# Kernel tuning notes

Measured on AMD Instinct MI355X. Metric: run time of the kernel, lower is better.

Reference implementation:

```python
import jax, jax.numpy as jnp
import numpy as np

M, A, E, H = 2048, 64, 128, 256
NUM_BOND_TYPES, NUM_ATOM_TYPES = 4, 118

def setup_inputs() -> dict:
    key = jax.random.key(0)
    ks = jax.random.split(key, 12)
    s = 0.02
    return {
        'node_rep': jax.random.normal(ks[0], (M, A, H), jnp.float32),
        'edge_index': jax.random.randint(ks[1], (M, 2, E), 0, A, jnp.int32),
        'bond_type_target': jax.random.randint(ks[2], (M, E), 0, NUM_BOND_TYPES, jnp.int32),
        'atom_type_target': jax.random.randint(ks[3], (M, A), 0, NUM_ATOM_TYPES, jnp.int32),
        'Wp1': jax.random.normal(ks[4], (H, H), jnp.float32) * s, 'bp1': jnp.zeros((H,), jnp.float32),
        'Wp2': jax.random.normal(ks[5], (H, H), jnp.float32) * s, 'bp2': jnp.zeros((H,), jnp.float32),
        'Wb1': jax.random.normal(ks[6], (2 * H, H), jnp.float32) * s, 'bb1': jnp.zeros((H,), jnp.float32),
        'Wb2': jax.random.normal(ks[7], (H, NUM_BOND_TYPES), jnp.float32) * s, 'bb2': jnp.zeros((NUM_BOND_TYPES,), jnp.float32),
        'Wa1': jax.random.normal(ks[8], (H, H), jnp.float32) * s, 'ba1': jnp.zeros((H,), jnp.float32),
        'Wa2': jax.random.normal(ks[9], (H, NUM_ATOM_TYPES), jnp.float32) * s, 'ba2': jnp.zeros((NUM_ATOM_TYPES,), jnp.float32),
    }

def _mlp(x, W1, b1, W2, b2):
    return jnp.maximum(x @ W1 + b1, 0.0) @ W2 + b2

def reference(node_rep, edge_index, bond_type_target, atom_type_target,
              Wp1, bp1, Wp2, bp2, Wb1, bb1, Wb2, bb2, Wa1, ba1, Wa2, ba2):
    # bond_if_proj: per-atom 2-layer MLP (dropout=0 -> identity)  [M,A,H]
    proj = _mlp(node_rep, Wp1, bp1, Wp2, bp2)
    # gather bond endpoint reps: index_select over atoms per molecule  [M,E,H]
    start = jnp.take_along_axis(proj, edge_index[:, 0, :, None], axis=1)
    end = jnp.take_along_axis(proj, edge_index[:, 1, :, None], axis=1)
    bt_in = jnp.concatenate([start, end], axis=-1)            # [M,E,2H]
    bt_logits = _mlp(bt_in, Wb1, bb1, Wb2, bb2)               # [M,E,4]
    bt_logp = jax.nn.log_softmax(bt_logits, axis=-1)
    # per-molecule mean CE averaged over molecules == global mean (equal sizes)
    bond_type_loss = -jnp.mean(jnp.take_along_axis(bt_logp, bond_type_target[..., None], axis=-1))
    bond_type_acc = jnp.mean((jnp.argmax(bt_logits, axis=-1) == bond_type_target).astype(jnp.float32))
    # atom type classifier on raw node reps  [M,A,118]
    at_logits = _mlp(node_rep, Wa1, ba1, Wa2, ba2)
    at_logp = jax.nn.log_softmax(at_logits, axis=-1)
    atom_type_loss = -jnp.mean(jnp.take_along_axis(at_logp, atom_type_target[..., None], axis=-1))
    atom_type_acc = jnp.mean((jnp.argmax(at_logits, axis=-1) == atom_type_target).astype(jnp.float32))
    loss = 0.5 * bond_type_loss + 0.5 * atom_type_loss
    return loss, bond_type_acc, atom_type_acc
```

## Files before the change

### kernel.cpp

```cpp
#include <hip/hip_runtime.h>
#include <hip/hip_bf16.h>

typedef __bf16 bf16x8 __attribute__((ext_vector_type(8)));
typedef float f32x16 __attribute__((ext_vector_type(16)));

__device__ inline unsigned short f2bf(float f) {
  __hip_bfloat16 h = __float2bfloat16(f);
  return *reinterpret_cast<unsigned short*>(&h);
}
__device__ inline unsigned pack2bf(float a, float b) {
  return (unsigned)f2bf(a) | ((unsigned)f2bf(b) << 16);
}
__device__ inline uint2 pack4bf(float a, float b, float c, float d) {
  uint2 r; r.x = pack2bf(a, b); r.y = pack2bf(c, d); return r;
}
__device__ inline bf16x8 as_bf16x8(uint4 v) { return __builtin_bit_cast(bf16x8, v); }
__device__ inline float bitf(unsigned u) { return __builtin_bit_cast(float, u); }
__device__ inline f32x16 mfma16(bf16x8 a, bf16x8 b, f32x16 c) {
  return __builtin_amdgcn_mfma_f32_32x32x16_bf16(a, b, c, 0, 0, 0);
}

#define BADDR(XB, R, KK)                                                       \
  ((XB) + (((((R) * 32 + l31) << 9) + ((KK) << 5) + (h << 4)) ^ swz))

#define GEMM22(XB, WPTR, CW_)                                                  \
  {                                                                            \
    const unsigned char* wb_ = (const unsigned char*)(WPTR) +                  \
                               (((CW_) + l31) << 5) + (h << 4);                \
    acc00 = zero; acc01 = zero; acc10 = zero; acc11 = zero;                    \
    bf16x8 pB0 = *(const bf16x8*)BADDR(XB, 0, 0);                              \
    bf16x8 pB1 = *(const bf16x8*)BADDR(XB, 1, 0);                              \
    uint4 pA0 = *(const uint4*)(wb_ + 0);                                      \
    uint4 pA1 = *(const uint4*)(wb_ + 1024);                                   \
    _Pragma("clang loop unroll(disable)")                                      \
    for (int kk = 0; kk < 16; kk += 2) {                                       \
      bf16x8 qB0 = *(const bf16x8*)BADDR(XB, 0, kk + 1);                       \
      bf16x8 qB1 = *(const bf16x8*)BADDR(XB, 1, kk + 1);                       \
      uint4 qA0 = *(const uint4*)(wb_ + ((kk + 1) << 13));                     \
      uint4 qA1 = *(const uint4*)(wb_ + ((kk + 1) << 13) + 1024);              \
      acc00 = mfma16(as_bf16x8(pA0), pB0, acc00);                              \
      acc10 = mfma16(as_bf16x8(pA1), pB0, acc10);                              \
      acc01 = mfma16(as_bf16x8(pA0), pB1, acc01);                              \
      acc11 = mfma16(as_bf16x8(pA1), pB1, acc11);                              \
      if (kk + 2 < 16) {                                                       \
        pB0 = *(const bf16x8*)BADDR(XB, 0, kk + 2);                            \
        pB1 = *(const bf16x8*)BADDR(XB, 1, kk + 2);                            \
        pA0 = *(const uint4*)(wb_ + ((kk + 2) << 13));                         \
        pA1 = *(const uint4*)(wb_ + ((kk + 2) << 13) + 1024);                  \
      }                                                                        \
      acc00 = mfma16(as_bf16x8(qA0), qB0, acc00);                              \
      acc10 = mfma16(as_bf16x8(qA1), qB0, acc10);                              \
      acc01 = mfma16(as_bf16x8(qA0), qB1, acc01);                              \
      acc11 = mfma16(as_bf16x8(qA1), qB1, acc11);                              \
    }                                                                          \
  }

#define WB22(DB, ACC, R, C, CW_, BIASPTR)                                      \
  _Pragma("unroll")                                                            \
  for (int g = 0; g < 4; ++g) {                                                \
    int xr_ = (R) * 32 + l31;                                                  \
    int col = (CW_) + (C) * 32 + g * 8 + h * 4;                                \
    float4 bb = *(const float4*)((BIASPTR) + col);                             \
    float v0 = fmaxf(ACC[4 * g + 0] + bb.x, 0.f);                              \
    float v1 = fmaxf(ACC[4 * g + 1] + bb.y, 0.f);                              \
    float v2 = fmaxf(ACC[4 * g + 2] + bb.z, 0.f);                              \
    float v3 = fmaxf(ACC[4 * g + 3] + bb.w, 0.f);                              \
    int off = ((xr_ << 9) + (col << 1)) ^ ((xr_ & 7) << 4);                    \
    *(uint2*)((DB) + off) = pack4bf(v0, v1, v2, v3);                           \
  }

#define WB22R(DB, ACC, R, C, CW_)                                              \
  _Pragma("unroll")                                                            \
  for (int g = 0; g < 4; ++g) {                                                \
    int xr_ = (R) * 32 + l31;                                                  \
    int col = (CW_) + (C) * 32 + g * 8 + h * 4;                                \
    int off = ((xr_ << 9) + (col << 1)) ^ ((xr_ & 7) << 4);                    \
    *(uint2*)((DB) + off) = pack4bf(ACC[4 * g + 0], ACC[4 * g + 1],            \
                                    ACC[4 * g + 2], ACC[4 * g + 3]);           \
  }

#define STAGE_X(DST, SRC)                                                      \
  _Pragma("unroll")                                                            \
  for (int it = 0; it < 8; ++it) {                                             \
    int lb = (it * 256 + tid) * 16;                                            \
    int d_ = lb ^ (((lb >> 9) & 7) << 4);                                      \
    const float4* s4 = (const float4*)((SRC) + (lb >> 1));                     \
    float4 f0 = s4[0], f1 = s4[1];                                             \
    uint4 v_ = { pack2bf(f0.x, f0.y), pack2bf(f0.z, f0.w),                     \
                 pack2bf(f1.x, f1.y), pack2bf(f1.z, f1.w) };                   \
    *(uint4*)((DST) + d_) = v_;                                                \
  }

__global__ __launch_bounds__(256) void k_pack(
    const float* __restrict__ wp1, const float* __restrict__ wa1,
    const float* __restrict__ wa2,
    unsigned short* __restrict__ dp1, unsigned short* __restrict__ da1,
    unsigned short* __restrict__ da2, float* __restrict__ accum)
{
  int b = blockIdx.x, tid = threadIdx.x;
  if (b == 0 && tid < 8) accum[tid] = 0.f;
  const float* src; unsigned short* dst; int e, logN, Nreal;
  if (b < 256)       { src = wp1; dst = dp1; e = b * 256 + tid;          logN = 8; Nreal = 256; }
  else if (b < 512)  { src = wa1; dst = da1; e = (b - 256) * 256 + tid;  logN = 8; Nreal = 256; }
  else               { src = wa2; dst = da2; e = (b - 512) * 256 + tid;  logN = 7; Nreal = 118; }
  int dk = e & 15;
  int rest = e >> 4;
  int n = rest & ((1 << logN) - 1);
  int kk = rest >> logN;
  int k = kk * 16 + dk;
  float v = (n < Nreal) ? src[k * Nreal + n] : 0.f;
  dst[e] = f2bf(v);
}

__global__ __launch_bounds__(256) void k_fold(
    const float* __restrict__ wp2, const float* __restrict__ wb1,
    const float* __restrict__ bp2, const float* __restrict__ bb1,
    unsigned short* __restrict__ dct, unsigned short* __restrict__ dcb,
    float* __restrict__ bias_e)
{
  int b = blockIdx.x, n = threadIdx.x;
  if (b < 512) {
    int k = b & 255;
    int off = (b < 256) ? 0 : 256;
    float s = 0.f;
    for (int t = 0; t < 256; ++t)
      s += wp2[k * 256 + t] * wb1[(t + off) * 256 + n];
    unsigned short* dst = (b < 256) ? dct : dcb;
    dst[((k >> 4) * 256 + n) * 16 + (k & 15)] = f2bf(s);
  } else {
    float s = bb1[n];
    for (int t = 0; t < 256; ++t)
      s += bp2[t] * (wb1[t * 256 + n] + wb1[(256 + t) * 256 + n]);
    bias_e[n] = s;
  }
}

__global__ __launch_bounds__(256, 2) void k_mol(
    const float* __restrict__ node, const int* __restrict__ eidx,
    const int* __restrict__ btt, const int* __restrict__ att,
    const unsigned short* __restrict__ wp1p, const float* __restrict__ bp1,
    const unsigned short* __restrict__ wctp, const unsigned short* __restrict__ wcbp,
    const float* __restrict__ bias_e, const float* __restrict__ wb2,
    const float* __restrict__ bb2,
    const unsigned short* __restrict__ wa1p, const float* __restrict__ ba1,
    const unsigned short* __restrict__ wa2p, const float* __restrict__ ba2,
    float* __restrict__ accum)
{
  __shared__ __align__(16) unsigned char bufA[32768];
  __shared__ __align__(16) unsigned char bufB[32768];
  __shared__ float s_bias[256];
  __shared__ float4 s_wb2[256];
  __shared__ float s_b2a[128];
  __shared__ float s_red[8];
  const int tid = threadIdx.x;
  const int lane = tid & 63;
  const int w = tid >> 6;
  const int l31 = lane & 31;
  const int h = lane >> 5;
  const int swz = (l31 & 7) << 4;
  const int CW = w * 64;
  const int m = blockIdx.x;

  STAGE_X(bufA, node + (long)m * 16384);
  s_bias[tid] = bias_e[tid];
  s_wb2[tid] = ((const float4*)wb2)[tid];
  if (tid < 128) s_b2a[tid] = (tid < 118) ? ba2[tid] : 0.f;
  __syncthreads();

  f32x16 zero = {};
  f32x16 acc00, acc01, acc10, acc11;

  GEMM22(bufA, wa1p, CW);
  WB22(bufB, acc00, 0, 0, CW, ba1);
  WB22(bufB, acc10, 0, 1, CW, ba1);
  WB22(bufB, acc01, 1, 0, CW, ba1);
  WB22(bufB, acc11, 1, 1, CW, ba1);
  __syncthreads();

  f32x16 accL0 = zero, accL1 = zero;
  {
    const int cw2 = w * 32;
    const unsigned char* wb_ = (const unsigned char*)wa2p +
                               ((cw2 + l31) << 5) + (h << 4);
    bf16x8 pB0 = *(const bf16x8*)BADDR(bufB, 0, 0);
    bf16x8 pB1 = *(const bf16x8*)BADDR(bufB, 1, 0);
    uint4 pA = *(const uint4*)(wb_);
    _Pragma("clang loop unroll(disable)")
    for (int kk = 0; kk < 16; kk += 2) {
      bf16x8 qB0 = *(const bf16x8*)BADDR(bufB, 0, kk + 1);
      bf16x8 qB1 = *(const bf16x8*)BADDR(bufB, 1, kk + 1);
      uint4 qA = *(const uint4*)(wb_ + ((kk + 1) << 12));
      accL0 = mfma16(as_bf16x8(pA), pB0, accL0);
      accL1 = mfma16(as_bf16x8(pA), pB1, accL1);
      if (kk + 2 < 16) {
        pB0 = *(const bf16x8*)BADDR(bufB, 0, kk + 2);
        pB1 = *(const bf16x8*)BADDR(bufB, 1, kk + 2);
        pA = *(const uint4*)(wb_ + ((kk + 2) << 12));
      }
      accL0 = mfma16(as_bf16x8(qA), qB0, accL0);
      accL1 = mfma16(as_bf16x8(qA), qB1, accL1);
    }
  }
  __syncthreads();

  {
    const int cw2 = w * 32;
    #pragma unroll
    for (int q = 0; q < 16; ++q) {
      int col = cw2 + (q & 3) + 8 * (q >> 2) + 4 * h;
      if (col < 118) {
        float bv = s_b2a[col];
        int r0 = l31, r1 = 32 + l31;
        *(float*)(bufB + ((r0 << 9) + (((col << 2)) ^ ((r0 & 7) << 4)))) = accL0[q] + bv;
        *(float*)(bufB + ((r1 << 9) + (((col << 2)) ^ ((r1 & 7) << 4)))) = accL1[q] + bv;
      }
    }
  }
  __syncthreads();

  {
    const int row = tid >> 2, g4 = tid & 3;
    const int t = att[m * 64 + row];
    const unsigned char* lr = bufB + (row << 9);
    const int rswz = (row & 7) << 4;
    const int c0 = g4 * 30;
    const int cend = (g4 == 3) ? 118 : c0 + 30;
    float mx = -3.0e38f; int am = 127;
    for (int c = c0; c < cend; ++c) {
      float v = *(const float*)(lr + (((c << 2)) ^ rswz));
      if (v > mx) { mx = v; am = c; }
    }
    float mo = __shfl_xor(mx, 1); int amo = __shfl_xor(am, 1);
    if (mo > mx || (mo == mx && amo < am)) { mx = mo; am = amo; }
    mo = __shfl_xor(mx, 2); amo = __shfl_xor(am, 2);
    if (mo > mx || (mo == mx && amo < am)) { mx = mo; am = amo; }
    float s = 0.f, vt = 0.f;
    for (int c = c0; c < cend; ++c) {
      float v = *(const float*)(lr + (((c << 2)) ^ rswz));
      s += __expf(v - mx);
      if (c == t) vt = v;
    }
    s += __shfl_xor(s, 1); s += __shfl_xor(s, 2);
    vt += __shfl_xor(vt, 1); vt += __shfl_xor(vt, 2);
    float ce = 0.f, cc = 0.f;
    if (g4 == 0) { ce = __logf(s) + mx - vt; cc = (am == t) ? 1.f : 0.f; }
    #pragma unroll
    for (int d = 1; d < 64; d <<= 1) { ce += __shfl_xor(ce, d); cc += __shfl_xor(cc, d); }
    if (lane == 0) { s_red[w * 2] = ce; s_red[w * 2 + 1] = cc; }
  }
  __syncthreads();
  if (tid == 0) {
    atomicAdd(accum + 2, s_red[0] + s_red[2] + s_red[4] + s_red[6]);
    atomicAdd(accum + 3, s_red[1] + s_red[3] + s_red[5] + s_red[7]);
  }

  GEMM22(bufA, wp1p, CW);
  WB22(bufB, acc00, 0, 0, CW, bp1);
  WB22(bufB, acc10, 0, 1, CW, bp1);
  WB22(bufB, acc01, 1, 0, CW, bp1);
  WB22(bufB, acc11, 1, 1, CW, bp1);
  __syncthreads();

  GEMM22(bufB, wctp, CW);
  WB22R(bufA, acc00, 0, 0, CW);
  WB22R(bufA, acc10, 0, 1, CW);
  WB22R(bufA, acc01, 1, 0, CW);
  WB22R(bufA, acc11, 1, 1, CW);
  GEMM22(bufB, wcbp, CW);
  const int es = eidx[m * 256 + (tid >> 1)];
  const int ed = eidx[m * 256 + 128 + (tid >> 1)];
  const int etg = btt[m * 128 + (tid >> 1)];
  const float b20 = bb2[0], b21 = bb2[1], b22 = bb2[2], b23 = bb2[3];
  __syncthreads();
  WB22R(bufB, acc00, 0, 0, CW);
  WB22R(bufB, acc10, 0, 1, CW);
  WB22R(bufB, acc01, 1, 0, CW);
  WB22R(bufB, acc11, 1, 1, CW);
  __syncthreads();

  {
    const int hf = tid & 1;
    float lg0 = 0.f, lg1 = 0.f, lg2 = 0.f, lg3 = 0.f;
    #pragma unroll
    for (int j = 0; j < 16; ++j) {
      int c0 = hf * 128 + j * 8;
      int offS = ((es << 9) + (c0 << 1)) ^ ((es & 7) << 4);
      int offD = ((ed << 9) + (c0 << 1)) ^ ((ed & 7) << 4);
      uint4 us = *(const uint4*)(bufA + offS);
      uint4 ud = *(const uint4*)(bufB + offD);
      const unsigned* pu = (const unsigned*)&us;
      const unsigned* pv = (const unsigned*)&ud;
      #pragma unroll
      for (int q = 0; q < 4; ++q) {
        unsigned ua = pu[q], ub = pv[q];
        int c = c0 + 2 * q;
        float hlo = bitf(ua << 16) + bitf(ub << 16) + s_bias[c];
        float hhi = bitf(ua & 0xffff0000u) + bitf(ub & 0xffff0000u) + s_bias[c + 1];
        hlo = fmaxf(hlo, 0.f); hhi = fmaxf(hhi, 0.f);
        float4 w0 = s_wb2[c], w1 = s_wb2[c + 1];
        lg0 = fmaf(hlo, w0.x, fmaf(hhi, w1.x, lg0));
        lg1 = fmaf(hlo, w0.y, fmaf(hhi, w1.y, lg1));
        lg2 = fmaf(hlo, w0.z, fmaf(hhi, w1.z, lg2));
        lg3 = fmaf(hlo, w0.w, fmaf(hhi, w1.w, lg3));
      }
    }
    lg0 += __shfl_xor(lg0, 1); lg1 += __shfl_xor(lg1, 1);
    lg2 += __shfl_xor(lg2, 1); lg3 += __shfl_xor(lg3, 1);
    float ce = 0.f, cc = 0.f;
    if (hf == 0) {
      float l0 = lg0 + b20, l1 = lg1 + b21, l2 = lg2 + b22, l3 = lg3 + b23;
      int t = etg;
      int am = 0; float mx = l0;
      if (l1 > mx) { mx = l1; am = 1; }
      if (l2 > mx) { mx = l2; am = 2; }
      if (l3 > mx) { mx = l3; am = 3; }
      float s = __expf(l0 - mx) + __expf(l1 - mx) + __expf(l2 - mx) + __expf(l3 - mx);
      float lt = (t == 0) ? l0 : (t == 1) ? l1 : (t == 2) ? l2 : l3;
      ce = __logf(s) + mx - lt;
      cc = (am == t) ? 1.f : 0.f;
    }
    #pragma unroll
    for (int d = 1; d < 64; d <<= 1) { ce += __shfl_xor(ce, d); cc += __shfl_xor(cc, d); }
    if (lane == 0) { s_red[w * 2] = ce; s_red[w * 2 + 1] = cc; }
    __syncthreads();
    if (tid == 0) {
      atomicAdd(accum + 0, s_red[0] + s_red[2] + s_red[4] + s_red[6]);
      atomicAdd(accum + 1, s_red[1] + s_red[3] + s_red[5] + s_red[7]);
    }
  }
}

__global__ __launch_bounds__(64) void k_final(const float* __restrict__ accum,
                                              float* __restrict__ out)
{
  if (threadIdx.x == 0) {
    float bce = accum[0] / 262144.f;
    float bcc = accum[1] / 262144.f;
    float ace = accum[2] / 131072.f;
    float acc_ = accum[3] / 131072.f;
    out[0] = 0.5f * bce + 0.5f * ace;
    out[1] = bcc;
    out[2] = acc_;
  }
}

extern "C" void kernel_launch(void* const* d_in, const int* in_sizes, int n_in,
                              void* d_out, int out_size, void* d_ws, size_t ws_size,
                              hipStream_t stream)
{
  const float* node = (const float*)d_in[0];
  const int* eidx   = (const int*)d_in[1];
  const int* btt    = (const int*)d_in[2];
  const int* att    = (const int*)d_in[3];
  const float* Wp1 = (const float*)d_in[4];
  const float* bp1 = (const float*)d_in[5];
  const float* Wp2 = (const float*)d_in[6];
  const float* bp2 = (const float*)d_in[7];
  const float* Wb1 = (const float*)d_in[8];
  const float* bb1 = (const float*)d_in[9];
  const float* Wb2 = (const float*)d_in[10];
  const float* bb2 = (const float*)d_in[11];
  const float* Wa1 = (const float*)d_in[12];
  const float* ba1 = (const float*)d_in[13];
  const float* Wa2 = (const float*)d_in[14];
  const float* ba2 = (const float*)d_in[15];

  char* ws = (char*)d_ws;
  float* accum = (float*)ws;
  unsigned short* dp1 = (unsigned short*)(ws + 256);
  unsigned short* da1 = (unsigned short*)(ws + 131328);
  unsigned short* da2 = (unsigned short*)(ws + 262400);
  unsigned short* dct = (unsigned short*)(ws + 327936);
  unsigned short* dcb = (unsigned short*)(ws + 459008);
  float* bias_e       = (float*)(ws + 590080);

  k_pack<<<640, 256, 0, stream>>>(Wp1, Wa1, Wa2, dp1, da1, da2, accum);
  k_fold<<<513, 256, 0, stream>>>(Wp2, Wb1, bp2, bb1, dct, dcb, bias_e);
  k_mol<<<2048, 256, 0, stream>>>(node, eidx, btt, att, dp1, bp1, dct, dcb,
                                  bias_e, Wb2, bb2, da1, ba1, da2, ba2, accum);
  k_final<<<1, 64, 0, stream>>>(accum, (float*)d_out);
}
```

Measured before the change: 195.4 us.

## Fuse paired GEMMs sharing the same LDS input into dual-weight MFMA loops

Merges the atom-head first layer with the projection first layer, and the two bond-endpoint projections, into one loop each. Each loop reads the shared LDS activation tile once and applies two weight matrices, so activation reads and loop overhead are halved and more independent MFMAs are in flight. The raw node tile in bufA is overwritten early by the projection output, which removes one GEMM phase and one barrier from the schedule. The cost is twice as many live accumulator registers (eight 16-float accumulators), which may reduce occupancy or cause spills.

```diff
diff --git a/kernel.cpp b/kernel.cpp
--- a/kernel.cpp
+++ b/kernel.cpp
@@ -23,35 +23,52 @@
 #define BADDR(XB, R, KK)                                                       \
   ((XB) + (((((R) * 32 + l31) << 9) + ((KK) << 5) + (h << 4)) ^ swz))
 
-#define GEMM22(XB, WPTR, CW_)                                                  \
+#define GEMMM(XB, W1PTR, W2PTR, CW_)                                           \
   {                                                                            \
-    const unsigned char* wb_ = (const unsigned char*)(WPTR) +                  \
+    const unsigned char* w1_ = (const unsigned char*)(W1PTR) +                 \
                                (((CW_) + l31) << 5) + (h << 4);                \
-    acc00 = zero; acc01 = zero; acc10 = zero; acc11 = zero;                    \
+    const unsigned char* w2_ = (const unsigned char*)(W2PTR) +                 \
+                               (((CW_) + l31) << 5) + (h << 4);                \
+    u00 = zero; u01 = zero; u10 = zero; u11 = zero;                            \
+    v00 = zero; v01 = zero; v10 = zero; v11 = zero;                            \
     bf16x8 pB0 = *(const bf16x8*)BADDR(XB, 0, 0);                              \
     bf16x8 pB1 = *(const bf16x8*)BADDR(XB, 1, 0);                              \
-    uint4 pA0 = *(const uint4*)(wb_ + 0);                                      \
-    uint4 pA1 = *(const uint4*)(wb_ + 1024);                                   \
+    uint4 pA0 = *(const uint4*)(w1_ + 0);                                      \
+    uint4 pA1 = *(const uint4*)(w1_ + 1024);                                   \
+    uint4 pC0 = *(const uint4*)(w2_ + 0);                                      \
+    uint4 pC1 = *(const uint4*)(w2_ + 1024);                                   \
     _Pragma("clang loop unroll(disable)")                                      \
     for (int kk = 0; kk < 16; kk += 2) {                                       \
       bf16x8 qB0 = *(const bf16x8*)BADDR(XB, 0, kk + 1);                       \
       bf16x8 qB1 = *(const bf16x8*)BADDR(XB, 1, kk + 1);                       \
-      uint4 qA0 = *(const uint4*)(wb_ + ((kk + 1) << 13));                     \
-      uint4 qA1 = *(const uint4*)(wb_ + ((kk + 1) << 13) + 1024);              \
-      acc00 = mfma16(as_bf16x8(pA0), pB0, acc00);                              \
-      acc10 = mfma16(as_bf16x8(pA1), pB0, acc10);                              \
-      acc01 = mfma16(as_bf16x8(pA0), pB1, acc01);                              \
-      acc11 = mfma16(as_bf16x8(pA1), pB1, acc11);                              \
+      uint4 qA0 = *(const uint4*)(w1_ + ((kk + 1) << 13));                     \
+      uint4 qA1 = *(const uint4*)(w1_ + ((kk + 1) << 13) + 1024);              \
+      uint4 qC0 = *(const uint4*)(w2_ + ((kk + 1) << 13));                     \
+      uint4 qC1 = *(const uint4*)(w2_ + ((kk + 1) << 13) + 1024);              \
+      u00 = mfma16(as_bf16x8(pA0), pB0, u00);                                  \
+      u10 = mfma16(as_bf16x8(pA1), pB0, u10);                                  \
+      u01 = mfma16(as_bf16x8(pA0), pB1, u01);                                  \
+      u11 = mfma16(as_bf16x8(pA1), pB1, u11);                                  \
+      v00 = mfma16(as_bf16x8(pC0), pB0, v00);                                  \
+      v10 = mfma16(as_bf16x8(pC1), pB0, v10);                                  \
+      v01 = mfma16(as_bf16x8(pC0), pB1, v01);                                  \
+      v11 = mfma16(as_bf16x8(pC1), pB1, v11);                                  \
       if (kk + 2 < 16) {                                                       \
         pB0 = *(const bf16x8*)BADDR(XB, 0, kk + 2);                            \
         pB1 = *(const bf16x8*)BADDR(XB, 1, kk + 2);                            \
-        pA0 = *(const uint4*)(wb_ + ((kk + 2) << 13));                         \
-        pA1 = *(const uint4*)(wb_ + ((kk + 2) << 13) + 1024);                  \
+        pA0 = *(const uint4*)(w1_ + ((kk + 2) << 13));                         \
+        pA1 = *(const uint4*)(w1_ + ((kk + 2) << 13) + 1024);                  \
+        pC0 = *(const uint4*)(w2_ + ((kk + 2) << 13));                         \
+        pC1 = *(const uint4*)(w2_ + ((kk + 2) << 13) + 1024);                  \
       }                                                                        \
-      acc00 = mfma16(as_bf16x8(qA0), qB0, acc00);                              \
-      acc10 = mfma16(as_bf16x8(qA1), qB0, acc10);                              \
-      acc01 = mfma16(as_bf16x8(qA0), qB1, acc01);                              \
-      acc11 = mfma16(as_bf16x8(qA1), qB1, acc11);                              \
+      u00 = mfma16(as_bf16x8(qA0), qB0, u00);                                  \
+      u10 = mfma16(as_bf16x8(qA1), qB0, u10);                                  \
+      u01 = mfma16(as_bf16x8(qA0), qB1, u01);                                  \
+      u11 = mfma16(as_bf16x8(qA1), qB1, u11);                                  \
+      v00 = mfma16(as_bf16x8(qC0), qB0, v00);                                  \
+      v10 = mfma16(as_bf16x8(qC1), qB0, v10);                                  \
+      v01 = mfma16(as_bf16x8(qC0), qB1, v01);                                  \
+      v11 = mfma16(as_bf16x8(qC1), qB1, v11);                                  \
     }                                                                          \
   }
 
@@ -165,16 +182,22 @@
   s_bias[tid] = bias_e[tid];
   s_wb2[tid] = ((const float4*)wb2)[tid];
   if (tid < 128) s_b2a[tid] = (tid < 118) ? ba2[tid] : 0.f;
+  const int t_at = att[m * 64 + (tid >> 2)];
   __syncthreads();
 
   f32x16 zero = {};
-  f32x16 acc00, acc01, acc10, acc11;
-
-  GEMM22(bufA, wa1p, CW);
-  WB22(bufB, acc00, 0, 0, CW, ba1);
-  WB22(bufB, acc10, 0, 1, CW, ba1);
-  WB22(bufB, acc01, 1, 0, CW, ba1);
-  WB22(bufB, acc11, 1, 1, CW, ba1);
+  f32x16 u00, u01, u10, u11, v00, v01, v10, v11;
+
+  GEMMM(bufA, wa1p, wp1p, CW);
+  WB22(bufB, u00, 0, 0, CW, ba1);
+  WB22(bufB, u10, 0, 1, CW, ba1);
+  WB22(bufB, u01, 1, 0, CW, ba1);
+  WB22(bufB, u11, 1, 1, CW, ba1);
+  __syncthreads();
+  WB22(bufA, v00, 0, 0, CW, bp1);
+  WB22(bufA, v10, 0, 1, CW, bp1);
+  WB22(bufA, v01, 1, 0, CW, bp1);
+  WB22(bufA, v11, 1, 1, CW, bp1);
   __syncthreads();
 
   f32x16 accL0 = zero, accL1 = zero;
@@ -220,7 +243,7 @@
 
   {
     const int row = tid >> 2, g4 = tid & 3;
-    const int t = att[m * 64 + row];
+    const int t = t_at;
     const unsigned char* lr = bufB + (row << 9);
     const int rswz = (row & 7) << 4;
     const int c0 = g4 * 30;
@@ -248,34 +271,25 @@
     for (int d = 1; d < 64; d <<= 1) { ce += __shfl_xor(ce, d); cc += __shfl_xor(cc, d); }
     if (lane == 0) { s_red[w * 2] = ce; s_red[w * 2 + 1] = cc; }
   }
-  __syncthreads();
-  if (tid == 0) {
-    atomicAdd(accum + 2, s_red[0] + s_red[2] + s_red[4] + s_red[6]);
-    atomicAdd(accum + 3, s_red[1] + s_red[3] + s_red[5] + s_red[7]);
-  }
-
-  GEMM22(bufA, wp1p, CW);
-  WB22(bufB, acc00, 0, 0, CW, bp1);
-  WB22(bufB, acc10, 0, 1, CW, bp1);
-  WB22(bufB, acc01, 1, 0, CW, bp1);
-  WB22(bufB, acc11, 1, 1, CW, bp1);
-  __syncthreads();
-
-  GEMM22(bufB, wctp, CW);
-  WB22R(bufA, acc00, 0, 0, CW);
-  WB22R(bufA, acc10, 0, 1, CW);
-  WB22R(bufA, acc01, 1, 0, CW);
-  WB22R(bufA, acc11, 1, 1, CW);
-  GEMM22(bufB, wcbp, CW);
+
+  GEMMM(bufA, wctp, wcbp, CW);
   const int es = eidx[m * 256 + (tid >> 1)];
   const int ed = eidx[m * 256 + 128 + (tid >> 1)];
   const int etg = btt[m * 128 + (tid >> 1)];
   const float b20 = bb2[0], b21 = bb2[1], b22 = bb2[2], b23 = bb2[3];
   __syncthreads();
-  WB22R(bufB, acc00, 0, 0, CW);
-  WB22R(bufB, acc10, 0, 1, CW);
-  WB22R(bufB, acc01, 1, 0, CW);
-  WB22R(bufB, acc11, 1, 1, CW);
+  if (tid == 0) {
+    atomicAdd(accum + 2, s_red[0] + s_red[2] + s_red[4] + s_red[6]);
+    atomicAdd(accum + 3, s_red[1] + s_red[3] + s_red[5] + s_red[7]);
+  }
+  WB22R(bufA, u00, 0, 0, CW);
+  WB22R(bufA, u10, 0, 1, CW);
+  WB22R(bufA, u01, 1, 0, CW);
+  WB22R(bufA, u11, 1, 1, CW);
+  WB22R(bufB, v00, 0, 0, CW);
+  WB22R(bufB, v10, 0, 1, CW);
+  WB22R(bufB, v01, 1, 0, CW);
+  WB22R(bufB, v11, 1, 1, CW);
   __syncthreads();
 
   {
```

After: 205.7 us. 5.3% more time.
